# Performance work log

Hardware: AMD Instinct MI355X
Metric: run time of the kernel (lower is better)

## Reference

```python
import jax, jax.numpy as jnp
import numpy as np

B, T, D, H = 2, 2048, 1024, 16
HS = D // H  # head_size = 64
EPS = 1e-5


def layer_norm(x, g, b):
    mu = jnp.mean(x, axis=-1, keepdims=True)
    var = jnp.var(x, axis=-1, keepdims=True)
    return (x - mu) * jax.lax.rsqrt(var + EPS) * g + b


def setup_inputs() -> dict:
    key = jax.random.key(0)
    ks = jax.random.split(key, 12)
    s_attn = 1.0 / np.sqrt(D)
    s_ff1 = 1.0 / np.sqrt(D)
    s_ff2 = 1.0 / np.sqrt(4 * D)
    return {
        "x": jax.random.normal(ks[0], (B, T, D), jnp.float32),
        "Wq": jax.random.normal(ks[1], (H, D, HS), jnp.float32) * s_attn,
        "Wk": jax.random.normal(ks[2], (H, D, HS), jnp.float32) * s_attn,
        "Wv": jax.random.normal(ks[3], (H, D, HS), jnp.float32) * s_attn,
        "Wo": jax.random.normal(ks[4], (H * HS, D), jnp.float32) * (1.0 / np.sqrt(H * HS)),
        "bo": jnp.zeros((D,), jnp.float32),
        "W1": jax.random.normal(ks[5], (D, 4 * D), jnp.float32) * s_ff1,
        "b1": jnp.zeros((4 * D,), jnp.float32),
        "W2": jax.random.normal(ks[6], (4 * D, D), jnp.float32) * s_ff2,
        "b2": jnp.zeros((D,), jnp.float32),
        "ln1_g": jnp.ones((D,), jnp.float32),
        "ln1_b": jnp.zeros((D,), jnp.float32),
        "ln2_g": jnp.ones((D,), jnp.float32),
        "ln2_b": jnp.zeros((D,), jnp.float32),
    }


def reference(x, Wq, Wk, Wv, Wo, bo, W1, b1, W2, b2, ln1_g, ln1_b, ln2_g, ln2_b):
    # --- self-attention on ln1(x) ---
    h = layer_norm(x, ln1_g, ln1_b)
    Q = jnp.einsum('bsd,hdk->bhsk', h, Wq)
    K = jnp.einsum('bsd,hdk->bhsk', h, Wk)
    V = jnp.einsum('bsd,hdk->bhsk', h, Wv)
    scores = jnp.einsum('bhqk,bhsk->bhqs', Q, K) * (HS ** -0.5)
    attn = jax.nn.softmax(scores, axis=-1)  # [B,H,T,T] non-causal, as in source
    out = jnp.einsum('bhqs,bhsk->bhqk', attn, V)
    out = out.transpose(0, 2, 1, 3).reshape(B, T, H * HS)  # concat heads
    sa = out @ Wo + bo
    x = x + sa
    # --- feed-forward on ln2(x) ---
    h2 = layer_norm(x, ln2_g, ln2_b)
    ff = jax.nn.relu(h2 @ W1 + b1) @ W2 + b2
    return x + ff
```

## Files before the change

kernel.cpp:

```cpp
#include <hip/hip_runtime.h>
#include <cstdint>
#include <cmath>

typedef __bf16 bf16;
typedef __bf16 bf16x8 __attribute__((ext_vector_type(8)));
typedef __bf16 bf16x4 __attribute__((ext_vector_type(4)));
typedef float  f32x4  __attribute__((ext_vector_type(4)));

#define B_   2
#define T_   2048
#define D_   1024
#define H_   16
#define HS_  64
#define NTOK (B_ * T_)

typedef __attribute__((address_space(1))) uint8_t* gp1_t;
typedef __attribute__((address_space(3))) uint8_t* lp3_t;
__device__ __forceinline__ void gl_lds16(const void* g, void* l) {
    __builtin_amdgcn_global_load_lds((gp1_t)(uintptr_t)g,
                                     (lp3_t)(uint32_t)(uintptr_t)l,
                                     16, 0, 0);
}

__device__ __forceinline__ f32x4 mfma16(bf16x8 a, bf16x8 b, f32x4 c) {
    return __builtin_amdgcn_mfma_f32_16x16x32_bf16(a, b, c, 0, 0, 0);
}

__global__ void tcast(const float* __restrict__ in, bf16* __restrict__ out,
                      int R, int C) {
    __shared__ float t[32][33];
    const int c0 = blockIdx.x * 32, r0 = blockIdx.y * 32;
    for (int i = 0; i < 4; i++) {
        int r = threadIdx.y + i * 8;
        t[r][threadIdx.x] = in[(size_t)(r0 + r) * C + c0 + threadIdx.x];
    }
    __syncthreads();
    for (int i = 0; i < 4; i++) {
        int rr = threadIdx.y + i * 8;
        out[(size_t)(c0 + rr) * R + r0 + threadIdx.x] = (bf16)t[threadIdx.x][rr];
    }
}

__global__ void qkv_pack(const float* __restrict__ Wq, const float* __restrict__ Wk,
                         const float* __restrict__ Wv, bf16* __restrict__ out) {
    const int z = blockIdx.z;
    const int qkv = z >> 4;
    const float* in = (qkv == 0 ? Wq : qkv == 1 ? Wk : Wv) + (size_t)(z & 15) * D_ * HS_;
    bf16* o = out + (size_t)z * HS_ * D_;
    __shared__ float t[32][33];
    const int c0 = blockIdx.x * 32, r0 = blockIdx.y * 32;
    for (int i = 0; i < 4; i++) {
        int r = threadIdx.y + i * 8;
        t[r][threadIdx.x] = in[(size_t)(r0 + r) * HS_ + c0 + threadIdx.x];
    }
    __syncthreads();
    for (int i = 0; i < 4; i++) {
        int rr = threadIdx.y + i * 8;
        o[(size_t)(c0 + rr) * D_ + r0 + threadIdx.x] = (bf16)t[threadIdx.x][rr];
    }
}

__global__ __launch_bounds__(256) void ln_kernel(const float* __restrict__ x,
                                                 const float* __restrict__ g,
                                                 const float* __restrict__ b,
                                                 bf16* __restrict__ out) {
    const int row = blockIdx.x;
    const int tid = threadIdx.x;
    const float4 v = ((const float4*)(x + (size_t)row * 1024))[tid];
    float s  = v.x + v.y + v.z + v.w;
    float s2 = v.x * v.x + v.y * v.y + v.z * v.z + v.w * v.w;
    for (int m = 1; m < 64; m <<= 1) {
        s  += __shfl_xor(s, m);
        s2 += __shfl_xor(s2, m);
    }
    __shared__ float rs[4], rq[4];
    const int lane = tid & 63, wv = tid >> 6;
    if (lane == 0) { rs[wv] = s; rq[wv] = s2; }
    __syncthreads();
    s  = rs[0] + rs[1] + rs[2] + rs[3];
    s2 = rq[0] + rq[1] + rq[2] + rq[3];
    const float mu   = s * (1.f / 1024.f);
    const float var  = s2 * (1.f / 1024.f) - mu * mu;
    const float rstd = rsqrtf(var + 1e-5f);
    const float4 gg = ((const float4*)g)[tid];
    const float4 bb = ((const float4*)b)[tid];
    bf16x4 o;
    o[0] = (bf16)((v.x - mu) * rstd * gg.x + bb.x);
    o[1] = (bf16)((v.y - mu) * rstd * gg.y + bb.y);
    o[2] = (bf16)((v.z - mu) * rstd * gg.z + bb.z);
    o[3] = (bf16)((v.w - mu) * rstd * gg.w + bb.w);
    *(bf16x4*)(out + (size_t)row * 1024 + tid * 4) = o;
}

__global__ __launch_bounds__(256) void combine2(const float* __restrict__ p0,
                                                const float* __restrict__ p1,
                                                const float* __restrict__ resid,
                                                const float* __restrict__ bias,
                                                float* __restrict__ out) {
    const int i4 = blockIdx.x * 256 + threadIdx.x;
    const float4 a = ((const float4*)p0)[i4];
    const float4 b = ((const float4*)p1)[i4];
    const float4 r = ((const float4*)resid)[i4];
    const float4 bb = ((const float4*)bias)[i4 & 255];
    float4 o;
    o.x = a.x + b.x + r.x + bb.x;
    o.y = a.y + b.y + r.y + bb.y;
    o.z = a.z + b.z + r.z + bb.z;
    o.w = a.w + b.w + r.w + bb.w;
    ((float4*)out)[i4] = o;
}

template <int BIAS, int RELU, int RES, int OUTBF16, int VTP = 0>
__global__ __launch_bounds__(256, 2) void gemm_bt(
    const bf16* __restrict__ A, const bf16* __restrict__ Bt,
    const float* __restrict__ bias, const float* __restrict__ resid,
    void* __restrict__ Cout, bf16* __restrict__ Vt, int M, int N, int K) {
    __shared__ __align__(16) bf16 As[2][128 * 32];
    __shared__ __align__(16) bf16 Bs[2][128 * 32];
    const int tid  = threadIdx.x;
    const int lane = tid & 63, w = tid >> 6;
    const int quad = lane >> 4, l15 = lane & 15;
    const int m0 = blockIdx.y * 128, n0 = blockIdx.x * 128;
    const int wm = (w & 1) * 64, wn = (w >> 1) * 64;

    f32x4 acc[4][4];
    for (int i = 0; i < 4; i++)
        for (int j = 0; j < 4; j++) acc[i][j] = f32x4{0.f, 0.f, 0.f, 0.f};

    const int arow = lane >> 2;
    const int acol = (lane & 3) * 8;
    const int c0 = w * 2, c1 = w * 2 + 1;

    for (int kt = 0; kt < K; kt += 64) {
        gl_lds16(A  + (size_t)(m0 + c0 * 16 + arow) * K + kt + acol,      &As[0][c0 * 512]);
        gl_lds16(A  + (size_t)(m0 + c1 * 16 + arow) * K + kt + acol,      &As[0][c1 * 512]);
        gl_lds16(A  + (size_t)(m0 + c0 * 16 + arow) * K + kt + 32 + acol, &As[1][c0 * 512]);
        gl_lds16(A  + (size_t)(m0 + c1 * 16 + arow) * K + kt + 32 + acol, &As[1][c1 * 512]);
        gl_lds16(Bt + (size_t)(n0 + c0 * 16 + arow) * K + kt + acol,      &Bs[0][c0 * 512]);
        gl_lds16(Bt + (size_t)(n0 + c1 * 16 + arow) * K + kt + acol,      &Bs[0][c1 * 512]);
        gl_lds16(Bt + (size_t)(n0 + c0 * 16 + arow) * K + kt + 32 + acol, &Bs[1][c0 * 512]);
        gl_lds16(Bt + (size_t)(n0 + c1 * 16 + arow) * K + kt + 32 + acol, &Bs[1][c1 * 512]);
        __syncthreads();
        for (int kh = 0; kh < 2; kh++) {
            bf16x8 af[4], bfr[4];
            for (int mi = 0; mi < 4; mi++)
                af[mi] = *(const bf16x8*)&As[kh][(wm + mi * 16 + l15) * 32 + quad * 8];
            for (int ni = 0; ni < 4; ni++)
                bfr[ni] = *(const bf16x8*)&Bs[kh][(wn + ni * 16 + l15) * 32 + quad * 8];
            for (int mi = 0; mi < 4; mi++)
                for (int ni = 0; ni < 4; ni++)
                    acc[mi][ni] = mfma16(af[mi], bfr[ni], acc[mi][ni]);
        }
        __syncthreads();
    }

    for (int mi = 0; mi < 4; mi++) {
        for (int ni = 0; ni < 4; ni++) {
            const int colb = n0 + wn + ni * 16 + l15;
            if (VTP && colb >= 2048) {
                const int h = (colb - 2048) >> 6, hs = (colb - 2048) & 63;
                const int row0 = m0 + wm + mi * 16 + quad * 4;
                const int b = row0 >> 11;
                bf16x4 p4;
                p4[0] = (bf16)acc[mi][ni][0];
                p4[1] = (bf16)acc[mi][ni][1];
                p4[2] = (bf16)acc[mi][ni][2];
                p4[3] = (bf16)acc[mi][ni][3];
                *(bf16x4*)&Vt[((size_t)(b * 16 + h) * 64 + hs) * T_ + (row0 & 2047)] = p4;
                continue;
            }
            const float bv = BIAS ? bias[colb] : 0.f;
            for (int r = 0; r < 4; r++) {
                const int row = m0 + wm + mi * 16 + quad * 4 + r;
                float v = acc[mi][ni][r] + bv;
                if (RELU) v = fmaxf(v, 0.f);
                if (RES)  v += resid[(size_t)row * N + colb];
                if (OUTBF16) ((bf16*)Cout)[(size_t)row * N + colb] = (bf16)v;
                else         ((float*)Cout)[(size_t)row * N + colb] = v;
            }
        }
    }
}

__global__ __launch_bounds__(256, 2) void gemm_bt_partial(
    const bf16* __restrict__ A, const bf16* __restrict__ Bt,
    float* __restrict__ Cpart, int M, int N, int K) {
    __shared__ __align__(16) bf16 As[2][128 * 32];
    __shared__ __align__(16) bf16 Bs[2][128 * 32];
    const int tid  = threadIdx.x;
    const int lane = tid & 63, w = tid >> 6;
    const int quad = lane >> 4, l15 = lane & 15;
    const int m0 = blockIdx.y * 128, n0 = blockIdx.x * 128;
    const int wm = (w & 1) * 64, wn = (w >> 1) * 64;
    const int kpb = K / gridDim.z;
    const int k0 = blockIdx.z * kpb, k1 = k0 + kpb;
    float* Cz = Cpart + (size_t)blockIdx.z * M * N;

    f32x4 acc[4][4];
    for (int i = 0; i < 4; i++)
        for (int j = 0; j < 4; j++) acc[i][j] = f32x4{0.f, 0.f, 0.f, 0.f};

    const int arow = lane >> 2;
    const int acol = (lane & 3) * 8;
    const int c0 = w * 2, c1 = w * 2 + 1;

    for (int kt = k0; kt < k1; kt += 64) {
        gl_lds16(A  + (size_t)(m0 + c0 * 16 + arow) * K + kt + acol,      &As[0][c0 * 512]);
        gl_lds16(A  + (size_t)(m0 + c1 * 16 + arow) * K + kt + acol,      &As[0][c1 * 512]);
        gl_lds16(A  + (size_t)(m0 + c0 * 16 + arow) * K + kt + 32 + acol, &As[1][c0 * 512]);
        gl_lds16(A  + (size_t)(m0 + c1 * 16 + arow) * K + kt + 32 + acol, &As[1][c1 * 512]);
        gl_lds16(Bt + (size_t)(n0 + c0 * 16 + arow) * K + kt + acol,      &Bs[0][c0 * 512]);
        gl_lds16(Bt + (size_t)(n0 + c1 * 16 + arow) * K + kt + acol,      &Bs[0][c1 * 512]);
        gl_lds16(Bt + (size_t)(n0 + c0 * 16 + arow) * K + kt + 32 + acol, &Bs[1][c0 * 512]);
        gl_lds16(Bt + (size_t)(n0 + c1 * 16 + arow) * K + kt + 32 + acol, &Bs[1][c1 * 512]);
        __syncthreads();
        for (int kh = 0; kh < 2; kh++) {
            bf16x8 af[4], bfr[4];
            for (int mi = 0; mi < 4; mi++)
                af[mi] = *(const bf16x8*)&As[kh][(wm + mi * 16 + l15) * 32 + quad * 8];
            for (int ni = 0; ni < 4; ni++)
                bfr[ni] = *(const bf16x8*)&Bs[kh][(wn + ni * 16 + l15) * 32 + quad * 8];
            for (int mi = 0; mi < 4; mi++)
                for (int ni = 0; ni < 4; ni++)
                    acc[mi][ni] = mfma16(af[mi], bfr[ni], acc[mi][ni]);
        }
        __syncthreads();
    }

    for (int mi = 0; mi < 4; mi++) {
        for (int ni = 0; ni < 4; ni++) {
            const int colb = n0 + wn + ni * 16 + l15;
            for (int r = 0; r < 4; r++) {
                const int row = m0 + wm + mi * 16 + quad * 4 + r;
                Cz[(size_t)row * N + colb] = acc[mi][ni][r];
            }
        }
    }
}

#define LSTR 68
#define NJ   (T_ / 64)
__global__ __launch_bounds__(256, 2) void flash_attn(const bf16* __restrict__ QKV,
                                                     const bf16* __restrict__ Vt,
                                                     bf16* __restrict__ attn_out) {
    const int bh = blockIdx.y, b = bh >> 4, h = bh & 15;
    const int q0 = blockIdx.x * 128;
    const int tid = threadIdx.x, lane = tid & 63, w = tid >> 6;
    const int quad = lane >> 4, l15 = lane & 15;
    __shared__ __align__(16) bf16 Ks[2][64 * LSTR];
    __shared__ __align__(16) bf16 Vs[2][64 * LSTR];
    __shared__ __align__(16) bf16 Ps[128 * LSTR];
    const bf16* Qb = QKV + (size_t)b * T_ * 3072 + h * 64;
    const bf16* Kb = QKV + (size_t)b * T_ * 3072 + 1024 + h * 64;
    const bf16* Vb = Vt  + (size_t)bh * HS_ * T_;

    const float sc = 0.125f * 1.44269504088896f;
    const int sr = tid >> 2, scc = (tid & 3) * 16;

    bf16x8 QA[2][2];
    for (int qnt = 0; qnt < 2; qnt++) {
        const size_t row = (size_t)(q0 + w * 32 + qnt * 16 + l15) * 3072;
        for (int kk = 0; kk < 2; kk++) {
            bf16x8 q = *(const bf16x8*)&Qb[row + kk * 32 + quad * 8];
            for (int i = 0; i < 8; i++) q[i] = (bf16)((float)q[i] * sc);
            QA[qnt][kk] = q;
        }
    }

    bf16x8 ones8;
    for (int i = 0; i < 8; i++) ones8[i] = (bf16)1.0f;

    f32x4 O[2][4], lacc[2];
    for (int mi = 0; mi < 2; mi++) {
        lacc[mi] = f32x4{0.f, 0.f, 0.f, 0.f};
        for (int n = 0; n < 4; n++) O[mi][n] = f32x4{0.f, 0.f, 0.f, 0.f};
    }

    *(bf16x8*)&Ks[0][sr * LSTR + scc]     = *(const bf16x8*)&Kb[(size_t)sr * 3072 + scc];
    *(bf16x8*)&Ks[0][sr * LSTR + scc + 8] = *(const bf16x8*)&Kb[(size_t)sr * 3072 + scc + 8];
    *(bf16x8*)&Vs[0][sr * LSTR + scc]     = *(const bf16x8*)&Vb[(size_t)sr * T_ + scc];
    *(bf16x8*)&Vs[0][sr * LSTR + scc + 8] = *(const bf16x8*)&Vb[(size_t)sr * T_ + scc + 8];
    __syncthreads();

    bf16x8 k0, k1, v0, v1;
    for (int j = 0; j < NJ; j++) {
        const int buf = j & 1;
        if (j + 1 < NJ) {
            const int s1 = (j + 1) * 64;
            k0 = *(const bf16x8*)&Kb[(size_t)(s1 + sr) * 3072 + scc];
            k1 = *(const bf16x8*)&Kb[(size_t)(s1 + sr) * 3072 + scc + 8];
            v0 = *(const bf16x8*)&Vb[(size_t)sr * T_ + s1 + scc];
            v1 = *(const bf16x8*)&Vb[(size_t)sr * T_ + s1 + scc + 8];
        }
        bf16x8 KB[4][2];
        for (int smt = 0; smt < 4; smt++)
            for (int kk = 0; kk < 2; kk++)
                KB[smt][kk] = *(const bf16x8*)&Ks[buf][(smt * 16 + l15) * LSTR + kk * 32 + quad * 8];
        for (int qnt = 0; qnt < 2; qnt++) {
            f32x4 ST[4];
            for (int smt = 0; smt < 4; smt++) ST[smt] = f32x4{0.f, 0.f, 0.f, 0.f};
            for (int kk = 0; kk < 2; kk++)
                for (int smt = 0; smt < 4; smt++)
                    ST[smt] = mfma16(KB[smt][kk], QA[qnt][kk], ST[smt]);
            const int prow = (w * 32 + qnt * 16 + l15) * LSTR + quad * 4;
            for (int smt = 0; smt < 4; smt++) {
                bf16x4 p4;
                p4[0] = (bf16)__builtin_amdgcn_exp2f(ST[smt][0]);
                p4[1] = (bf16)__builtin_amdgcn_exp2f(ST[smt][1]);
                p4[2] = (bf16)__builtin_amdgcn_exp2f(ST[smt][2]);
                p4[3] = (bf16)__builtin_amdgcn_exp2f(ST[smt][3]);
                *(bf16x4*)&Ps[prow + smt * 16] = p4;
            }
        }
        bf16x8 VB[4][2];
        for (int n = 0; n < 4; n++)
            for (int kk = 0; kk < 2; kk++)
                VB[n][kk] = *(const bf16x8*)&Vs[buf][(n * 16 + l15) * LSTR + kk * 32 + quad * 8];
        for (int mi = 0; mi < 2; mi++) {
            const int pr = (w * 32 + mi * 16 + l15) * LSTR + quad * 8;
            bf16x8 PA0 = *(const bf16x8*)&Ps[pr];
            bf16x8 PA1 = *(const bf16x8*)&Ps[pr + 32];
            for (int n = 0; n < 4; n++) {
                O[mi][n] = mfma16(PA0, VB[n][0], O[mi][n]);
                O[mi][n] = mfma16(PA1, VB[n][1], O[mi][n]);
            }
            lacc[mi] = mfma16(PA0, ones8, lacc[mi]);
            lacc[mi] = mfma16(PA1, ones8, lacc[mi]);
        }
        if (j + 1 < NJ) {
            *(bf16x8*)&Ks[buf ^ 1][sr * LSTR + scc]     = k0;
            *(bf16x8*)&Ks[buf ^ 1][sr * LSTR + scc + 8] = k1;
            *(bf16x8*)&Vs[buf ^ 1][sr * LSTR + scc]     = v0;
            *(bf16x8*)&Vs[buf ^ 1][sr * LSTR + scc + 8] = v1;
        }
        __syncthreads();
    }

    for (int mi = 0; mi < 2; mi++) {
        for (int r = 0; r < 4; r++) {
            const float inv = 1.f / lacc[mi][r];
            const size_t tok = (size_t)b * T_ + q0 + w * 32 + mi * 16 + quad * 4 + r;
            for (int n = 0; n < 4; n++)
                attn_out[tok * 1024 + h * 64 + n * 16 + l15] = (bf16)(O[mi][n][r] * inv);
        }
    }
}

extern "C" void kernel_launch(void* const* d_in, const int* in_sizes, int n_in,
                              void* d_out, int out_size, void* d_ws, size_t ws_size,
                              hipStream_t stream) {
    const float* x   = (const float*)d_in[0];
    const float* Wq  = (const float*)d_in[1];
    const float* Wk  = (const float*)d_in[2];
    const float* Wv  = (const float*)d_in[3];
    const float* Wo  = (const float*)d_in[4];
    const float* bo  = (const float*)d_in[5];
    const float* W1  = (const float*)d_in[6];
    const float* b1  = (const float*)d_in[7];
    const float* W2  = (const float*)d_in[8];
    const float* b2  = (const float*)d_in[9];
    const float* g1  = (const float*)d_in[10];
    const float* be1 = (const float*)d_in[11];
    const float* g2  = (const float*)d_in[12];
    const float* be2 = (const float*)d_in[13];

    char* ws = (char*)d_ws;
    const size_t MB = 1ull << 20;
    bf16*  WqkvT = (bf16*)(ws);
    bf16*  WoT   = (bf16*)(ws + 6  * MB);
    bf16*  W1T   = (bf16*)(ws + 8  * MB);
    bf16*  W2T   = (bf16*)(ws + 16 * MB);
    bf16*  hbuf  = (bf16*)(ws + 24 * MB);
    bf16*  QKV   = (bf16*)(ws + 32 * MB);
    bf16*  Vt    = (bf16*)(ws + 56 * MB);
    bf16*  attn  = (bf16*)(ws + 64 * MB);
    float* x2    = (float*)(ws + 72 * MB);
    bf16*  ff1   = (bf16*)(ws + 32 * MB);
    float* part  = (float*)(ws + 88 * MB);
    float* out   = (float*)d_out;

    dim3 tb(32, 8);
    qkv_pack<<<dim3(2, 32, 48), tb, 0, stream>>>(Wq, Wk, Wv, WqkvT);
    tcast<<<dim3(32, 32),  tb, 0, stream>>>(Wo, WoT, 1024, 1024);
    tcast<<<dim3(128, 32), tb, 0, stream>>>(W1, W1T, 1024, 4096);
    tcast<<<dim3(32, 128), tb, 0, stream>>>(W2, W2T, 4096, 1024);
    ln_kernel<<<NTOK, 256, 0, stream>>>(x, g1, be1, hbuf);
    gemm_bt<0, 0, 0, 1, 1><<<dim3(24, 32), 256, 0, stream>>>(hbuf, WqkvT, nullptr, nullptr, QKV, Vt, NTOK, 3072, 1024);
    flash_attn<<<dim3(T_ / 128, B_ * H_), 256, 0, stream>>>(QKV, Vt, attn);
    gemm_bt<1, 0, 1, 0><<<dim3(8, 32), 256, 0, stream>>>(attn, WoT, bo, x, x2, nullptr, NTOK, 1024, 1024);
    ln_kernel<<<NTOK, 256, 0, stream>>>(x2, g2, be2, hbuf);
    gemm_bt<1, 1, 0, 1><<<dim3(32, 32), 256, 0, stream>>>(hbuf, W1T, b1, nullptr, ff1, nullptr, NTOK, 4096, 1024);
    gemm_bt_partial<<<dim3(8, 32, 2), 256, 0, stream>>>(ff1, W2T, part, NTOK, 1024, 4096);
    combine2<<<NTOK, 256, 0, stream>>>(part, part + (size_t)NTOK * 1024, x2, b2, out);
}
```

Before: 340.3 us.

## Split attention over the key dimension and split-K the output projection

Flash attention now splits the key range into two halves via a third grid dimension. Each half writes unnormalized fp32 partial outputs and row sums, and a new combine kernel sums the halves and normalizes. The kernel drops to single-buffered K/V LDS with a higher occupancy hint. The Wo projection now uses the split-K partial GEMM plus combine2, and the GEMM grids are transposed so the M tiles run along blockIdx.x. The intent is more parallel blocks and better occupancy for attention, at the cost of extra fp32 partial-buffer traffic and two more kernel launches.

```diff
diff --git a/kernel.cpp b/kernel.cpp
--- a/kernel.cpp
+++ b/kernel.cpp
@@ -110,6 +110,27 @@
     ((float4*)out)[i4] = o;
 }
 
+__global__ __launch_bounds__(256) void attn_combine(const float* __restrict__ Opart,
+                                                    const float* __restrict__ lpart,
+                                                    bf16* __restrict__ attn) {
+    const int i4 = blockIdx.x * 256 + threadIdx.x;
+    const int tok = i4 >> 8;
+    const int c = (i4 & 255) * 4;
+    const int h = c >> 6;
+    const int b = tok >> 11, t = tok & 2047;
+    const int bh = b * 16 + h;
+    const float l = lpart[(size_t)bh * T_ + t] + lpart[(size_t)(32 + bh) * T_ + t];
+    const float inv = 1.f / l;
+    const float4 o0 = ((const float4*)Opart)[i4];
+    const float4 o1 = ((const float4*)Opart)[(size_t)NTOK * 256 + i4];
+    bf16x4 o;
+    o[0] = (bf16)((o0.x + o1.x) * inv);
+    o[1] = (bf16)((o0.y + o1.y) * inv);
+    o[2] = (bf16)((o0.z + o1.z) * inv);
+    o[3] = (bf16)((o0.w + o1.w) * inv);
+    *(bf16x4*)&attn[(size_t)tok * 1024 + c] = o;
+}
+
 template <int BIAS, int RELU, int RES, int OUTBF16, int VTP = 0>
 __global__ __launch_bounds__(256, 2) void gemm_bt(
     const bf16* __restrict__ A, const bf16* __restrict__ Bt,
@@ -120,7 +141,7 @@
     const int tid  = threadIdx.x;
     const int lane = tid & 63, w = tid >> 6;
     const int quad = lane >> 4, l15 = lane & 15;
-    const int m0 = blockIdx.y * 128, n0 = blockIdx.x * 128;
+    const int m0 = blockIdx.x * 128, n0 = blockIdx.y * 128;
     const int wm = (w & 1) * 64, wn = (w >> 1) * 64;
 
     f32x4 acc[4][4];
@@ -190,7 +211,7 @@
     const int tid  = threadIdx.x;
     const int lane = tid & 63, w = tid >> 6;
     const int quad = lane >> 4, l15 = lane & 15;
-    const int m0 = blockIdx.y * 128, n0 = blockIdx.x * 128;
+    const int m0 = blockIdx.x * 128, n0 = blockIdx.y * 128;
     const int wm = (w & 1) * 64, wn = (w >> 1) * 64;
     const int kpb = K / gridDim.z;
     const int k0 = blockIdx.z * kpb, k1 = k0 + kpb;
@@ -239,16 +260,19 @@
 }
 
 #define LSTR 68
-#define NJ   (T_ / 64)
-__global__ __launch_bounds__(256, 2) void flash_attn(const bf16* __restrict__ QKV,
+#define NJH  (T_ / 64 / 2)
+__global__ __launch_bounds__(256, 4) void flash_attn(const bf16* __restrict__ QKV,
                                                      const bf16* __restrict__ Vt,
-                                                     bf16* __restrict__ attn_out) {
+                                                     float* __restrict__ Opart,
+                                                     float* __restrict__ lpart) {
     const int bh = blockIdx.y, b = bh >> 4, h = bh & 15;
     const int q0 = blockIdx.x * 128;
+    const int z = blockIdx.z;
+    const int jbeg = z * NJH;
     const int tid = threadIdx.x, lane = tid & 63, w = tid >> 6;
     const int quad = lane >> 4, l15 = lane & 15;
-    __shared__ __align__(16) bf16 Ks[2][64 * LSTR];
-    __shared__ __align__(16) bf16 Vs[2][64 * LSTR];
+    __shared__ __align__(16) bf16 Ks[64 * LSTR];
+    __shared__ __align__(16) bf16 Vs[64 * LSTR];
     __shared__ __align__(16) bf16 Ps[128 * LSTR];
     const bf16* Qb = QKV + (size_t)b * T_ * 3072 + h * 64;
     const bf16* Kb = QKV + (size_t)b * T_ * 3072 + 1024 + h * 64;
@@ -276,17 +300,24 @@
         for (int n = 0; n < 4; n++) O[mi][n] = f32x4{0.f, 0.f, 0.f, 0.f};
     }
 
-    *(bf16x8*)&Ks[0][sr * LSTR + scc]     = *(const bf16x8*)&Kb[(size_t)sr * 3072 + scc];
-    *(bf16x8*)&Ks[0][sr * LSTR + scc + 8] = *(const bf16x8*)&Kb[(size_t)sr * 3072 + scc + 8];
-    *(bf16x8*)&Vs[0][sr * LSTR + scc]     = *(const bf16x8*)&Vb[(size_t)sr * T_ + scc];
-    *(bf16x8*)&Vs[0][sr * LSTR + scc + 8] = *(const bf16x8*)&Vb[(size_t)sr * T_ + scc + 8];
-    __syncthreads();
-
     bf16x8 k0, k1, v0, v1;
-    for (int j = 0; j < NJ; j++) {
-        const int buf = j & 1;
-        if (j + 1 < NJ) {
-            const int s1 = (j + 1) * 64;
+    {
+        const int s0 = jbeg * 64;
+        k0 = *(const bf16x8*)&Kb[(size_t)(s0 + sr) * 3072 + scc];
+        k1 = *(const bf16x8*)&Kb[(size_t)(s0 + sr) * 3072 + scc + 8];
+        v0 = *(const bf16x8*)&Vb[(size_t)sr * T_ + s0 + scc];
+        v1 = *(const bf16x8*)&Vb[(size_t)sr * T_ + s0 + scc + 8];
+    }
+
+    for (int jj = 0; jj < NJH; jj++) {
+        __syncthreads();
+        *(bf16x8*)&Ks[sr * LSTR + scc]     = k0;
+        *(bf16x8*)&Ks[sr * LSTR + scc + 8] = k1;
+        *(bf16x8*)&Vs[sr * LSTR + scc]     = v0;
+        *(bf16x8*)&Vs[sr * LSTR + scc + 8] = v1;
+        __syncthreads();
+        if (jj + 1 < NJH) {
+            const int s1 = (jbeg + jj + 1) * 64;
             k0 = *(const bf16x8*)&Kb[(size_t)(s1 + sr) * 3072 + scc];
             k1 = *(const bf16x8*)&Kb[(size_t)(s1 + sr) * 3072 + scc + 8];
             v0 = *(const bf16x8*)&Vb[(size_t)sr * T_ + s1 + scc];
@@ -295,7 +326,7 @@
         bf16x8 KB[4][2];
         for (int smt = 0; smt < 4; smt++)
             for (int kk = 0; kk < 2; kk++)
-                KB[smt][kk] = *(const bf16x8*)&Ks[buf][(smt * 16 + l15) * LSTR + kk * 32 + quad * 8];
+                KB[smt][kk] = *(const bf16x8*)&Ks[(smt * 16 + l15) * LSTR + kk * 32 + quad * 8];
         for (int qnt = 0; qnt < 2; qnt++) {
             f32x4 ST[4];
             for (int smt = 0; smt < 4; smt++) ST[smt] = f32x4{0.f, 0.f, 0.f, 0.f};
@@ -315,7 +346,7 @@
         bf16x8 VB[4][2];
         for (int n = 0; n < 4; n++)
             for (int kk = 0; kk < 2; kk++)
-                VB[n][kk] = *(const bf16x8*)&Vs[buf][(n * 16 + l15) * LSTR + kk * 32 + quad * 8];
+                VB[n][kk] = *(const bf16x8*)&Vs[(n * 16 + l15) * LSTR + kk * 32 + quad * 8];
         for (int mi = 0; mi < 2; mi++) {
             const int pr = (w * 32 + mi * 16 + l15) * LSTR + quad * 8;
             bf16x8 PA0 = *(const bf16x8*)&Ps[pr];
@@ -327,22 +358,17 @@
             lacc[mi] = mfma16(PA0, ones8, lacc[mi]);
             lacc[mi] = mfma16(PA1, ones8, lacc[mi]);
         }
-        if (j + 1 < NJ) {
-            *(bf16x8*)&Ks[buf ^ 1][sr * LSTR + scc]     = k0;
-            *(bf16x8*)&Ks[buf ^ 1][sr * LSTR + scc + 8] = k1;
-            *(bf16x8*)&Vs[buf ^ 1][sr * LSTR + scc]     = v0;
-            *(bf16x8*)&Vs[buf ^ 1][sr * LSTR + scc + 8] = v1;
-        }
-        __syncthreads();
-    }
-
+    }
+
+    float* Oz = Opart + (size_t)z * NTOK * 1024;
     for (int mi = 0; mi < 2; mi++) {
         for (int r = 0; r < 4; r++) {
-            const float inv = 1.f / lacc[mi][r];
             const size_t tok = (size_t)b * T_ + q0 + w * 32 + mi * 16 + quad * 4 + r;
             for (int n = 0; n < 4; n++)
-                attn_out[tok * 1024 + h * 64 + n * 16 + l15] = (bf16)(O[mi][n][r] * inv);
-        }
+                Oz[tok * 1024 + h * 64 + n * 16 + l15] = O[mi][n][r];
+        }
+        if (l15 == 0)
+            *(f32x4*)&lpart[((size_t)z * 32 + bh) * T_ + q0 + w * 32 + mi * 16 + quad * 4] = lacc[mi];
     }
 }
 
@@ -374,6 +400,7 @@
     bf16*  QKV   = (bf16*)(ws + 32 * MB);
     bf16*  Vt    = (bf16*)(ws + 56 * MB);
     bf16*  attn  = (bf16*)(ws + 64 * MB);
+    float* lpart = (float*)(ws + 72 * MB);
     float* x2    = (float*)(ws + 72 * MB);
     bf16*  ff1   = (bf16*)(ws + 32 * MB);
     float* part  = (float*)(ws + 88 * MB);
@@ -385,11 +412,13 @@
     tcast<<<dim3(128, 32), tb, 0, stream>>>(W1, W1T, 1024, 4096);
     tcast<<<dim3(32, 128), tb, 0, stream>>>(W2, W2T, 4096, 1024);
     ln_kernel<<<NTOK, 256, 0, stream>>>(x, g1, be1, hbuf);
-    gemm_bt<0, 0, 0, 1, 1><<<dim3(24, 32), 256, 0, stream>>>(hbuf, WqkvT, nullptr, nullptr, QKV, Vt, NTOK, 3072, 1024);
-    flash_attn<<<dim3(T_ / 128, B_ * H_), 256, 0, stream>>>(QKV, Vt, attn);
-    gemm_bt<1, 0, 1, 0><<<dim3(8, 32), 256, 0, stream>>>(attn, WoT, bo, x, x2, nullptr, NTOK, 1024, 1024);
+    gemm_bt<0, 0, 0, 1, 1><<<dim3(32, 24), 256, 0, stream>>>(hbuf, WqkvT, nullptr, nullptr, QKV, Vt, NTOK, 3072, 1024);
+    flash_attn<<<dim3(T_ / 128, B_ * H_, 2), 256, 0, stream>>>(QKV, Vt, part, lpart);
+    attn_combine<<<NTOK * 4, 256, 0, stream>>>(part, lpart, attn);
+    gemm_bt_partial<<<dim3(32, 8, 2), 256, 0, stream>>>(attn, WoT, part, NTOK, 1024, 1024);
+    combine2<<<NTOK, 256, 0, stream>>>(part, part + (size_t)NTOK * 1024, x, bo, x2);
     ln_kernel<<<NTOK, 256, 0, stream>>>(x2, g2, be2, hbuf);
     gemm_bt<1, 1, 0, 1><<<dim3(32, 32), 256, 0, stream>>>(hbuf, W1T, b1, nullptr, ff1, nullptr, NTOK, 4096, 1024);
-    gemm_bt_partial<<<dim3(8, 32, 2), 256, 0, stream>>>(ff1, W2T, part, NTOK, 1024, 4096);
+    gemm_bt_partial<<<dim3(32, 8, 2), 256, 0, stream>>>(ff1, W2T, part, NTOK, 1024, 4096);
     combine2<<<NTOK, 256, 0, stream>>>(part, part + (size_t)NTOK * 1024, x2, b2, out);
 }
```

After: 366.3 us. 1.08x slower.

## Split key range across two warp groups in flash attention with LDS reduction

Applied to the files above, without the earlier changes.

Doubles the attention block to 512 threads, with each half of the warps processing half of the key sequence for the same 128 queries. At the end the partial outputs and row sums are combined through shared memory. The aim is more waves in flight and a shorter sequential loop per block. In exchange, K/V double buffering is replaced by single buffering with two barriers per iteration, and LDS per block grows.

```diff
diff --git a/kernel.cpp b/kernel.cpp
--- a/kernel.cpp
+++ b/kernel.cpp
@@ -239,27 +239,31 @@
 }
 
 #define LSTR 68
-#define NJ   (T_ / 64)
-__global__ __launch_bounds__(256, 2) void flash_attn(const bf16* __restrict__ QKV,
+#define NJH  16
+__global__ __launch_bounds__(512, 4) void flash_attn(const bf16* __restrict__ QKV,
                                                      const bf16* __restrict__ Vt,
                                                      bf16* __restrict__ attn_out) {
     const int bh = blockIdx.y, b = bh >> 4, h = bh & 15;
     const int q0 = blockIdx.x * 128;
     const int tid = threadIdx.x, lane = tid & 63, w = tid >> 6;
+    const int sh = w >> 2, wq = w & 3;
     const int quad = lane >> 4, l15 = lane & 15;
-    __shared__ __align__(16) bf16 Ks[2][64 * LSTR];
-    __shared__ __align__(16) bf16 Vs[2][64 * LSTR];
-    __shared__ __align__(16) bf16 Ps[128 * LSTR];
+    __shared__ __align__(16) bf16 smem[34816];
+    bf16* Ks = smem + sh * 4352;
+    bf16* Vs = smem + 8704 + sh * 4352;
+    bf16* Ps = smem + 17408 + sh * 8704;
     const bf16* Qb = QKV + (size_t)b * T_ * 3072 + h * 64;
     const bf16* Kb = QKV + (size_t)b * T_ * 3072 + 1024 + h * 64;
     const bf16* Vb = Vt  + (size_t)bh * HS_ * T_;
 
     const float sc = 0.125f * 1.44269504088896f;
-    const int sr = tid >> 2, scc = (tid & 3) * 16;
+    const int lt = tid & 255;
+    const int sr = lt >> 2, scc = (lt & 3) * 16;
+    const int jbeg = sh * NJH;
 
     bf16x8 QA[2][2];
     for (int qnt = 0; qnt < 2; qnt++) {
-        const size_t row = (size_t)(q0 + w * 32 + qnt * 16 + l15) * 3072;
+        const size_t row = (size_t)(q0 + wq * 32 + qnt * 16 + l15) * 3072;
         for (int kk = 0; kk < 2; kk++) {
             bf16x8 q = *(const bf16x8*)&Qb[row + kk * 32 + quad * 8];
             for (int i = 0; i < 8; i++) q[i] = (bf16)((float)q[i] * sc);
@@ -276,17 +280,24 @@
         for (int n = 0; n < 4; n++) O[mi][n] = f32x4{0.f, 0.f, 0.f, 0.f};
     }
 
-    *(bf16x8*)&Ks[0][sr * LSTR + scc]     = *(const bf16x8*)&Kb[(size_t)sr * 3072 + scc];
-    *(bf16x8*)&Ks[0][sr * LSTR + scc + 8] = *(const bf16x8*)&Kb[(size_t)sr * 3072 + scc + 8];
-    *(bf16x8*)&Vs[0][sr * LSTR + scc]     = *(const bf16x8*)&Vb[(size_t)sr * T_ + scc];
-    *(bf16x8*)&Vs[0][sr * LSTR + scc + 8] = *(const bf16x8*)&Vb[(size_t)sr * T_ + scc + 8];
-    __syncthreads();
-
     bf16x8 k0, k1, v0, v1;
-    for (int j = 0; j < NJ; j++) {
-        const int buf = j & 1;
-        if (j + 1 < NJ) {
-            const int s1 = (j + 1) * 64;
+    {
+        const int s0 = jbeg * 64;
+        k0 = *(const bf16x8*)&Kb[(size_t)(s0 + sr) * 3072 + scc];
+        k1 = *(const bf16x8*)&Kb[(size_t)(s0 + sr) * 3072 + scc + 8];
+        v0 = *(const bf16x8*)&Vb[(size_t)sr * T_ + s0 + scc];
+        v1 = *(const bf16x8*)&Vb[(size_t)sr * T_ + s0 + scc + 8];
+    }
+
+    for (int jj = 0; jj < NJH; jj++) {
+        __syncthreads();
+        *(bf16x8*)&Ks[sr * LSTR + scc]     = k0;
+        *(bf16x8*)&Ks[sr * LSTR + scc + 8] = k1;
+        *(bf16x8*)&Vs[sr * LSTR + scc]     = v0;
+        *(bf16x8*)&Vs[sr * LSTR + scc + 8] = v1;
+        __syncthreads();
+        if (jj + 1 < NJH) {
+            const int s1 = (jbeg + jj + 1) * 64;
             k0 = *(const bf16x8*)&Kb[(size_t)(s1 + sr) * 3072 + scc];
             k1 = *(const bf16x8*)&Kb[(size_t)(s1 + sr) * 3072 + scc + 8];
             v0 = *(const bf16x8*)&Vb[(size_t)sr * T_ + s1 + scc];
@@ -295,14 +306,14 @@
         bf16x8 KB[4][2];
         for (int smt = 0; smt < 4; smt++)
             for (int kk = 0; kk < 2; kk++)
-                KB[smt][kk] = *(const bf16x8*)&Ks[buf][(smt * 16 + l15) * LSTR + kk * 32 + quad * 8];
+                KB[smt][kk] = *(const bf16x8*)&Ks[(smt * 16 + l15) * LSTR + kk * 32 + quad * 8];
         for (int qnt = 0; qnt < 2; qnt++) {
             f32x4 ST[4];
             for (int smt = 0; smt < 4; smt++) ST[smt] = f32x4{0.f, 0.f, 0.f, 0.f};
             for (int kk = 0; kk < 2; kk++)
                 for (int smt = 0; smt < 4; smt++)
                     ST[smt] = mfma16(KB[smt][kk], QA[qnt][kk], ST[smt]);
-            const int prow = (w * 32 + qnt * 16 + l15) * LSTR + quad * 4;
+            const int prow = (wq * 32 + qnt * 16 + l15) * LSTR + quad * 4;
             for (int smt = 0; smt < 4; smt++) {
                 bf16x4 p4;
                 p4[0] = (bf16)__builtin_amdgcn_exp2f(ST[smt][0]);
@@ -315,9 +326,9 @@
         bf16x8 VB[4][2];
         for (int n = 0; n < 4; n++)
             for (int kk = 0; kk < 2; kk++)
-                VB[n][kk] = *(const bf16x8*)&Vs[buf][(n * 16 + l15) * LSTR + kk * 32 + quad * 8];
+                VB[n][kk] = *(const bf16x8*)&Vs[(n * 16 + l15) * LSTR + kk * 32 + quad * 8];
         for (int mi = 0; mi < 2; mi++) {
-            const int pr = (w * 32 + mi * 16 + l15) * LSTR + quad * 8;
+            const int pr = (wq * 32 + mi * 16 + l15) * LSTR + quad * 8;
             bf16x8 PA0 = *(const bf16x8*)&Ps[pr];
             bf16x8 PA1 = *(const bf16x8*)&Ps[pr + 32];
             for (int n = 0; n < 4; n++) {
@@ -327,21 +338,31 @@
             lacc[mi] = mfma16(PA0, ones8, lacc[mi]);
             lacc[mi] = mfma16(PA1, ones8, lacc[mi]);
         }
-        if (j + 1 < NJ) {
-            *(bf16x8*)&Ks[buf ^ 1][sr * LSTR + scc]     = k0;
-            *(bf16x8*)&Ks[buf ^ 1][sr * LSTR + scc + 8] = k1;
-            *(bf16x8*)&Vs[buf ^ 1][sr * LSTR + scc]     = v0;
-            *(bf16x8*)&Vs[buf ^ 1][sr * LSTR + scc + 8] = v1;
-        }
-        __syncthreads();
-    }
-
-    for (int mi = 0; mi < 2; mi++) {
-        for (int r = 0; r < 4; r++) {
-            const float inv = 1.f / lacc[mi][r];
-            const size_t tok = (size_t)b * T_ + q0 + w * 32 + mi * 16 + quad * 4 + r;
+    }
+
+    __syncthreads();
+    float* fscr = (float*)smem;
+    const int idx = (wq * 64 + lane) * 40;
+    if (sh == 1) {
+        for (int mi = 0; mi < 2; mi++)
             for (int n = 0; n < 4; n++)
-                attn_out[tok * 1024 + h * 64 + n * 16 + l15] = (bf16)(O[mi][n][r] * inv);
+                *(f32x4*)&fscr[idx + (mi * 4 + n) * 4] = O[mi][n];
+        *(f32x4*)&fscr[idx + 32] = lacc[0];
+        *(f32x4*)&fscr[idx + 36] = lacc[1];
+    }
+    __syncthreads();
+    if (sh == 0) {
+        for (int mi = 0; mi < 2; mi++) {
+            const f32x4 lo = *(const f32x4*)&fscr[idx + 32 + mi * 4];
+            for (int r = 0; r < 4; r++) {
+                const float inv = 1.f / (lacc[mi][r] + lo[r]);
+                const size_t tok = (size_t)b * T_ + q0 + wq * 32 + mi * 16 + quad * 4 + r;
+                for (int n = 0; n < 4; n++) {
+                    const float oo = fscr[idx + (mi * 4 + n) * 4 + r];
+                    attn_out[tok * 1024 + h * 64 + n * 16 + l15] =
+                        (bf16)((O[mi][n][r] + oo) * inv);
+                }
+            }
         }
     }
 }
@@ -386,7 +407,7 @@
     tcast<<<dim3(32, 128), tb, 0, stream>>>(W2, W2T, 4096, 1024);
     ln_kernel<<<NTOK, 256, 0, stream>>>(x, g1, be1, hbuf);
     gemm_bt<0, 0, 0, 1, 1><<<dim3(24, 32), 256, 0, stream>>>(hbuf, WqkvT, nullptr, nullptr, QKV, Vt, NTOK, 3072, 1024);
-    flash_attn<<<dim3(T_ / 128, B_ * H_), 256, 0, stream>>>(QKV, Vt, attn);
+    flash_attn<<<dim3(T_ / 128, B_ * H_), 512, 0, stream>>>(QKV, Vt, attn);
     gemm_bt<1, 0, 1, 0><<<dim3(8, 32), 256, 0, stream>>>(attn, WoT, bo, x, x2, nullptr, NTOK, 1024, 1024);
     ln_kernel<<<NTOK, 256, 0, stream>>>(x2, g2, be2, hbuf);
     gemm_bt<1, 1, 0, 1><<<dim3(32, 32), 256, 0, stream>>>(hbuf, W1T, b1, nullptr, ff1, nullptr, NTOK, 4096, 1024);
```

Measured after the change: 472.4 us. 38.8% more time.
